# Performance work log

Hardware: AMD Instinct MI355X
Metric: run time of the kernel (lower is better)

## Reference

```python
import jax, jax.numpy as jnp
import numpy as np

N_NODES = 50000
N_EDGES = 800000
F_IN, D1, N_CLS = 128, 128, 64


def gcn_conv(x, W, b, src, dst, n):
    # x: [N, Fin] -> linear transform then normalized scatter-add aggregation
    h = x @ W  # [N, Fout]
    deg = jnp.zeros((n,), h.dtype).at[dst].add(jnp.ones((dst.shape[0],), h.dtype))
    dis = jnp.where(deg > 0, jax.lax.rsqrt(jnp.maximum(deg, 1.0)), 0.0)  # deg^-1/2, inf->0
    norm = dis[src] * dis[dst]  # [E_tot]
    msgs = norm[:, None] * h[src]  # gather source features, scale by sym norm
    out = jax.ops.segment_sum(msgs, dst, num_segments=n)  # scatter-add to targets
    return out + b


def setup_inputs() -> dict:
    key = jax.random.key(0)
    ks = jax.random.split(key, 6)
    x = jax.random.normal(ks[0], (N_NODES, F_IN), dtype=jnp.float32)
    edge_index = jax.random.randint(ks[1], (2, N_EDGES), 0, N_NODES, dtype=jnp.int64)
    W1 = jax.random.normal(ks[2], (F_IN, D1), dtype=jnp.float32) / np.sqrt(F_IN)
    b1 = jnp.zeros((D1,), dtype=jnp.float32)
    W2 = jax.random.normal(ks[3], (D1, N_CLS), dtype=jnp.float32) / np.sqrt(D1)
    b2 = jnp.zeros((N_CLS,), dtype=jnp.float32)
    return {"x": x, "edge_index": edge_index, "W1": W1, "b1": b1, "W2": W2, "b2": b2}


def reference(x, edge_index, W1, b1, W2, b2):
    n = x.shape[0]
    loops = jnp.arange(n, dtype=edge_index.dtype)
    src = jnp.concatenate([edge_index[0], loops])  # add self-loops (PyG default)
    dst = jnp.concatenate([edge_index[1], loops])
    h = gcn_conv(x, W1, b1, src, dst, n)
    h = jax.nn.relu(h)
    # F.dropout(training=self.training) is identity in eval mode
    out = gcn_conv(h, W2, b2, src, dst, n)
    return out
```

## Files before the change

kernel.cpp:

```cpp
#include <hip/hip_runtime.h>
#include <hip/hip_fp16.h>

#define NN 50000
#define NE 800000
#define CAP 64
#define CSTR 32
#define SLICE 6250

typedef unsigned int   u32;
typedef unsigned short u16;
typedef __attribute__((ext_vector_type(8))) short short8;
typedef __attribute__((ext_vector_type(4))) float f32x4;

__device__ inline u16 f2bf(float f) {
    u32 u = __float_as_uint(f);
    return (u16)((u + 0x7FFF + ((u >> 16) & 1)) >> 16);
}
__device__ inline float bfval(u16 h) { return __uint_as_float(((u32)h) << 16); }
__device__ inline float bf_lo(u32 u) { return __uint_as_float(u << 16); }
__device__ inline float bf_hi(u32 u) { return __uint_as_float(u & 0xFFFF0000u); }


__global__ __launch_bounds__(256) void build_ell(const int* __restrict__ ei,
                                                 int* __restrict__ cnt,
                                                 u16* __restrict__ ell) {
    const int s = blockIdx.x & 7;
    const int g = blockIdx.x >> 3;
    const int u = g * 256 + (int)threadIdx.x;
    const int lo = s * SLICE, hi = lo + SLICE;

    int dv[16], sv[16];
#pragma unroll
    for (int k = 0; k < 4; ++k) {
        int e0 = (u + k * 51200) * 4;
        if (e0 < NE) {
            *(int4*)&dv[k * 4] = *(const int4*)(ei + NE + e0);
            *(int4*)&sv[k * 4] = *(const int4*)(ei + e0);
        } else {
#pragma unroll
            for (int j = 0; j < 4; ++j) { dv[k * 4 + j] = -1; sv[k * 4 + j] = 0; }
        }
    }

    int pos[16];
#pragma unroll
    for (int k = 0; k < 16; ++k) {
        pos[k] = -1;
        if (dv[k] >= lo && dv[k] < hi)
            pos[k] = atomicAdd(&cnt[(size_t)dv[k] * CSTR], 1);
    }
#pragma unroll
    for (int k = 0; k < 16; ++k)
        if (pos[k] >= 0 && pos[k] < CAP)
            ell[(size_t)dv[k] * CAP + pos[k]] = (u16)sv[k];
}


__global__ __launch_bounds__(256) void prep_w(const float* __restrict__ W1,
                                              const float* __restrict__ W2,
                                              u16* __restrict__ W1h, u16* __restrict__ W1l,
                                              u16* __restrict__ W2h, u16* __restrict__ W2l,
                                              int* __restrict__ cnt) {
    int i = blockIdx.x * 256 + threadIdx.x;
    int4* c4 = (int4*)cnt;
    const int4 z = make_int4(0, 0, 0, 0);
    for (int v = i; v < NN * CSTR / 4; v += 32768) c4[v] = z;
    const float* W; u16 *Dh, *Dl; int NOUT, idx;
    if (i < 16384) { W = W1; Dh = W1h; Dl = W1l; NOUT = 128; idx = i; }
    else           { idx = i - 16384; if (idx >= 8192) return;
                     W = W2; Dh = W2h; Dl = W2l; NOUT = 64; }
    int j = idx & 7, l = (idx >> 3) & 63, kc = (idx >> 9) & 3, t = idx >> 11;
    int k = kc * 32 + (l >> 4) * 8 + j;
    int n = t * 16 + (l & 15);
    float w = W[k * NOUT + n];
    u16 h = f2bf(w);
    Dh[idx] = h;
    Dl[idx] = f2bf(w - bfval(h));
}


__global__ __launch_bounds__(256) void pack_edges(const u16* __restrict__ ell,
                                                  const int* __restrict__ cnt,
                                                  u32* __restrict__ epk,
                                                  u16* __restrict__ degm) {
    const int tid = threadIdx.x;
    const int node = blockIdx.x * 4 + (tid >> 6);
    if (node >= NN) return;
    const int lane = tid & 63;
    const int cr = cnt[(size_t)node * CSTR];
    const int ne = min(cr, 63);
    const float di = rsqrtf((float)(cr + 1));
    if (lane == 0) degm[node] = (u16)(ne + 1);
    if (lane > ne) return;
    int s; float nr;
    if (lane < ne) {
        s = (int)ell[(size_t)node * CAP + lane];
        nr = rsqrtf((float)(cnt[(size_t)s * CSTR] + 1)) * di;
    } else { s = node; nr = di * di; }
    epk[(size_t)node * CAP + lane] =
        (u32)s | ((u32)__half_as_ushort(__float2half_rn(nr)) << 16);
}


__global__ __launch_bounds__(256) void gemm1(const float* __restrict__ A,
                                             const u16* __restrict__ Wh,
                                             const u16* __restrict__ Wl,
                                             u16* __restrict__ C) {
    const int tid = threadIdx.x;
    const int w = tid >> 6, l = tid & 63;
    const int m = l & 15, q = l >> 4;

    int arow = blockIdx.x * 64 + w * 16 + m;
    const float* Ar = A + (size_t)min(arow, NN - 1) * 128;

    f32x4 acc[8] = {};
#pragma unroll
    for (int kc = 0; kc < 4; ++kc) {
        float p[8];
        *(float4*)&p[0] = *(const float4*)(Ar + kc * 32 + q * 8);
        *(float4*)&p[4] = *(const float4*)(Ar + kc * 32 + q * 8 + 4);
        short8 ah, al;
#pragma unroll
        for (int j = 0; j < 8; ++j) {
            u16 h = f2bf(p[j]);
            ah[j] = (short)h;
            al[j] = (short)f2bf(p[j] - bfval(h));
        }
#pragma unroll
        for (int t2 = 0; t2 < 8; ++t2) {
            size_t bo = ((size_t)(t2 * 4 + kc) * 64 + l) * 8;
            short8 bh = *(const short8*)(Wh + bo);
            short8 bl = *(const short8*)(Wl + bo);
            acc[t2] = __builtin_amdgcn_mfma_f32_16x16x32_bf16(ah, bh, acc[t2], 0, 0, 0);
            acc[t2] = __builtin_amdgcn_mfma_f32_16x16x32_bf16(al, bh, acc[t2], 0, 0, 0);
            acc[t2] = __builtin_amdgcn_mfma_f32_16x16x32_bf16(ah, bl, acc[t2], 0, 0, 0);
        }
    }
    int growbase = blockIdx.x * 64 + w * 16 + q * 4;
#pragma unroll
    for (int t2 = 0; t2 < 8; ++t2)
#pragma unroll
        for (int r = 0; r < 4; ++r) {
            int grow = growbase + r;
            if (grow < NN) C[(size_t)grow * 128 + t2 * 16 + m] = f2bf(acc[t2][r]);
        }
}


__global__ __launch_bounds__(256) void gemm2(const u16* __restrict__ A,
                                             const u16* __restrict__ Wh,
                                             const u16* __restrict__ Wl,
                                             u16* __restrict__ C) {
    const int tid = threadIdx.x;
    const int w = tid >> 6, l = tid & 63;
    const int m = l & 15, q = l >> 4;

    int arow = min(blockIdx.x * 64 + w * 16 + m, NN - 1);
    const u16* Ar = A + (size_t)arow * 128;

    f32x4 acc[4] = {};
#pragma unroll
    for (int kc = 0; kc < 4; ++kc) {
        short8 ah = *(const short8*)(Ar + kc * 32 + q * 8);
#pragma unroll
        for (int t2 = 0; t2 < 4; ++t2) {
            size_t bo = ((size_t)(t2 * 4 + kc) * 64 + l) * 8;
            short8 bh = *(const short8*)(Wh + bo);
            short8 bl = *(const short8*)(Wl + bo);
            acc[t2] = __builtin_amdgcn_mfma_f32_16x16x32_bf16(ah, bh, acc[t2], 0, 0, 0);
            acc[t2] = __builtin_amdgcn_mfma_f32_16x16x32_bf16(ah, bl, acc[t2], 0, 0, 0);
        }
    }
    int growbase = blockIdx.x * 64 + w * 16 + q * 4;
#pragma unroll
    for (int t2 = 0; t2 < 4; ++t2)
#pragma unroll
        for (int r = 0; r < 4; ++r) {
            int grow = growbase + r;
            if (grow < NN) C[(size_t)grow * 64 + t2 * 16 + m] = f2bf(acc[t2][r]);
        }
}


template <int F, bool RELU, bool OUTBF>
__global__ __launch_bounds__(256) void aggregate(const u16* __restrict__ H,
                                                 const u32* __restrict__ epk,
                                                 const u16* __restrict__ degm,
                                                 const float* __restrict__ bias,
                                                 void* __restrict__ outp) {
    const int tid = threadIdx.x;
    const int node = (int)((blockIdx.x * 256 + tid) >> 6);
    if (node >= NN) return;
    const int lane = tid & 63;

    const int m = (int)degm[node];
    u32 e = (lane < m) ? epk[(size_t)node * CAP + lane] : (u32)node;
    int   s_l = (int)(e & 0xFFFF);
    float n_l = (lane < m)
                    ? __half2float(__ushort_as_half((u16)(e >> 16)))
                    : 0.0f;

    constexpr int G = (F == 128) ? 4 : 8;
    constexpr int L = 64 / G;
    const int g = lane / L;
    const int ci = lane & (L - 1);

    const int mPad = (m + 2 * G - 1) & ~(2 * G - 1);

    float acc[8] = {0, 0, 0, 0, 0, 0, 0, 0};
    for (int j = 0; j < mPad; j += 2 * G) {
        int   sA = __shfl(s_l, j + g);
        float nA = __shfl(n_l, j + g);
        int   sB = __shfl(s_l, j + G + g);
        float nB = __shfl(n_l, j + G + g);
        uint4 vA = *(const uint4*)(H + (size_t)sA * F + ci * 8);
        uint4 vB = *(const uint4*)(H + (size_t)sB * F + ci * 8);
        acc[0] += nA * bf_lo(vA.x); acc[1] += nA * bf_hi(vA.x);
        acc[2] += nA * bf_lo(vA.y); acc[3] += nA * bf_hi(vA.y);
        acc[4] += nA * bf_lo(vA.z); acc[5] += nA * bf_hi(vA.z);
        acc[6] += nA * bf_lo(vA.w); acc[7] += nA * bf_hi(vA.w);
        acc[0] += nB * bf_lo(vB.x); acc[1] += nB * bf_hi(vB.x);
        acc[2] += nB * bf_lo(vB.y); acc[3] += nB * bf_hi(vB.y);
        acc[4] += nB * bf_lo(vB.z); acc[5] += nB * bf_hi(vB.z);
        acc[6] += nB * bf_lo(vB.w); acc[7] += nB * bf_hi(vB.w);
    }

#pragma unroll
    for (int i = 0; i < 8; ++i) {
        if (F == 64) acc[i] += __shfl_xor(acc[i], 8);
        acc[i] += __shfl_xor(acc[i], 16);
        acc[i] += __shfl_xor(acc[i], 32);
    }

    const int active = (F == 128) ? 32 : 16;
    if (lane < active) {
        int part, c0i;
        if (F == 128) { part = lane >> 4;       c0i = (lane & 15) * 8 + part * 4; }
        else          { part = (lane >> 3) & 1; c0i = (lane & 7) * 8 + part * 4; }
        float4 b4 = *(const float4*)(bias + c0i);
        float4 o = make_float4(acc[part * 4 + 0] + b4.x, acc[part * 4 + 1] + b4.y,
                               acc[part * 4 + 2] + b4.z, acc[part * 4 + 3] + b4.w);
        if (RELU) { o.x = fmaxf(o.x, 0.f); o.y = fmaxf(o.y, 0.f);
                    o.z = fmaxf(o.z, 0.f); o.w = fmaxf(o.w, 0.f); }
        if (OUTBF) {
            u16* out = (u16*)outp;
            *(ushort4*)(out + (size_t)node * F + c0i) =
                make_ushort4(f2bf(o.x), f2bf(o.y), f2bf(o.z), f2bf(o.w));
        } else {
            float* out = (float*)outp;
            *(float4*)(out + (size_t)node * F + c0i) = o;
        }
    }
}


extern "C" void kernel_launch(void* const* d_in, const int* in_sizes, int n_in,
                              void* d_out, int out_size, void* d_ws, size_t ws_size,
                              hipStream_t stream) {
    const float* x  = (const float*)d_in[0];
    const int*   ei = (const int*)d_in[1];
    const float* W1 = (const float*)d_in[2];
    const float* b1 = (const float*)d_in[3];
    const float* W2 = (const float*)d_in[4];
    const float* b2 = (const float*)d_in[5];
    float* out = (float*)d_out;

    char* ws = (char*)d_ws;
    size_t off = 0;
    int* cnt = (int*)ws;                     off += (size_t)NN * CSTR * 4;
    u16* ell = (u16*)(ws + off);             off += (size_t)NN * CAP * 2;
    off = (off + 255) & ~(size_t)255;
    u32* epk = (u32*)(ws + off);             off += (size_t)NN * CAP * 4;
    u16* degm = (u16*)(ws + off);            off += (size_t)NN * 2;
    off = (off + 255) & ~(size_t)255;
    u16* W1h = (u16*)(ws + off);             off += 16384 * 2;
    u16* W1l = (u16*)(ws + off);             off += 16384 * 2;
    u16* W2h = (u16*)(ws + off);             off += 8192 * 2;
    u16* W2l = (u16*)(ws + off);             off += 8192 * 2;
    off = (off + 255) & ~(size_t)255;
    u16* Hbf = (u16*)(ws + off);             off += (size_t)NN * 128 * 2;
    u16* Abf = (u16*)(ws + off);             off += (size_t)NN * 128 * 2;

    prep_w<<<128, 256, 0, stream>>>(W1, W2, W1h, W1l, W2h, W2l, cnt);
    build_ell<<<1600, 256, 0, stream>>>(ei, cnt, ell);
    pack_edges<<<12500, 256, 0, stream>>>(ell, cnt, epk, degm);

    gemm1<<<(NN + 63) / 64, 256, 0, stream>>>(x, W1h, W1l, Hbf);
    aggregate<128, true, true><<<(NN + 3) / 4, 256, 0, stream>>>(Hbf, epk, degm, b1, Abf);

    gemm2<<<(NN + 63) / 64, 256, 0, stream>>>(Abf, W2h, W2l, Hbf);
    aggregate<64, false, false><<<(NN + 3) / 4, 256, 0, stream>>>(Hbf, epk, degm, b2, out);
}
```

Measured before the change: 213.2 us.

## Fuse graph build with gemm1 and edge packing with layer-1 aggregation

Runs the independent ELL build and the first GEMM in one launch by splitting the grid into GEMM blocks and build blocks. The edge-packing pass is folded into the first aggregation kernel, which computes normalisation coefficients itself while still writing the packed edges for layer 2. The goal is to remove two kernel launches and one extra read of ell/cnt, and to let GEMM work overlap with the atomic-heavy build. In exchange the fused kernels carry more register pressure and a mixed per-block workload.

New measurement: 196.9 us. -7.6%, faster.

```diff
diff --git a/kernel.cpp b/kernel.cpp
--- a/kernel.cpp
+++ b/kernel.cpp
@@ -6,6 +6,7 @@
 #define CAP 64
 #define CSTR 32
 #define SLICE 6250
+#define GT1 782
 
 typedef unsigned int   u32;
 typedef unsigned short u16;
@@ -19,41 +20,6 @@
 __device__ inline float bfval(u16 h) { return __uint_as_float(((u32)h) << 16); }
 __device__ inline float bf_lo(u32 u) { return __uint_as_float(u << 16); }
 __device__ inline float bf_hi(u32 u) { return __uint_as_float(u & 0xFFFF0000u); }
-
-
-__global__ __launch_bounds__(256) void build_ell(const int* __restrict__ ei,
-                                                 int* __restrict__ cnt,
-                                                 u16* __restrict__ ell) {
-    const int s = blockIdx.x & 7;
-    const int g = blockIdx.x >> 3;
-    const int u = g * 256 + (int)threadIdx.x;
-    const int lo = s * SLICE, hi = lo + SLICE;
-
-    int dv[16], sv[16];
-#pragma unroll
-    for (int k = 0; k < 4; ++k) {
-        int e0 = (u + k * 51200) * 4;
-        if (e0 < NE) {
-            *(int4*)&dv[k * 4] = *(const int4*)(ei + NE + e0);
-            *(int4*)&sv[k * 4] = *(const int4*)(ei + e0);
-        } else {
-#pragma unroll
-            for (int j = 0; j < 4; ++j) { dv[k * 4 + j] = -1; sv[k * 4 + j] = 0; }
-        }
-    }
-
-    int pos[16];
-#pragma unroll
-    for (int k = 0; k < 16; ++k) {
-        pos[k] = -1;
-        if (dv[k] >= lo && dv[k] < hi)
-            pos[k] = atomicAdd(&cnt[(size_t)dv[k] * CSTR], 1);
-    }
-#pragma unroll
-    for (int k = 0; k < 16; ++k)
-        if (pos[k] >= 0 && pos[k] < CAP)
-            ell[(size_t)dv[k] * CAP + pos[k]] = (u16)sv[k];
-}
 
 
 __global__ __launch_bounds__(256) void prep_w(const float* __restrict__ W1,
@@ -79,38 +45,46 @@
 }
 
 
-__global__ __launch_bounds__(256) void pack_edges(const u16* __restrict__ ell,
-                                                  const int* __restrict__ cnt,
-                                                  u32* __restrict__ epk,
-                                                  u16* __restrict__ degm) {
-    const int tid = threadIdx.x;
-    const int node = blockIdx.x * 4 + (tid >> 6);
-    if (node >= NN) return;
-    const int lane = tid & 63;
-    const int cr = cnt[(size_t)node * CSTR];
-    const int ne = min(cr, 63);
-    const float di = rsqrtf((float)(cr + 1));
-    if (lane == 0) degm[node] = (u16)(ne + 1);
-    if (lane > ne) return;
-    int s; float nr;
-    if (lane < ne) {
-        s = (int)ell[(size_t)node * CAP + lane];
-        nr = rsqrtf((float)(cnt[(size_t)s * CSTR] + 1)) * di;
-    } else { s = node; nr = di * di; }
-    epk[(size_t)node * CAP + lane] =
-        (u32)s | ((u32)__half_as_ushort(__float2half_rn(nr)) << 16);
-}
-
-
-__global__ __launch_bounds__(256) void gemm1(const float* __restrict__ A,
-                                             const u16* __restrict__ Wh,
-                                             const u16* __restrict__ Wl,
-                                             u16* __restrict__ C) {
-    const int tid = threadIdx.x;
+__device__ void dev_build(int b, int tid, const int* __restrict__ ei,
+                          int* __restrict__ cnt, u16* __restrict__ ell) {
+    const int s = b & 7;
+    const int g = b >> 3;
+    const int u = g * 256 + tid;
+    const int lo = s * SLICE, hi = lo + SLICE;
+
+    int dv[16], sv[16];
+#pragma unroll
+    for (int k = 0; k < 4; ++k) {
+        int e0 = (u + k * 51200) * 4;
+        if (e0 < NE) {
+            *(int4*)&dv[k * 4] = *(const int4*)(ei + NE + e0);
+            *(int4*)&sv[k * 4] = *(const int4*)(ei + e0);
+        } else {
+#pragma unroll
+            for (int j = 0; j < 4; ++j) { dv[k * 4 + j] = -1; sv[k * 4 + j] = 0; }
+        }
+    }
+
+    int pos[16];
+#pragma unroll
+    for (int k = 0; k < 16; ++k) {
+        pos[k] = -1;
+        if (dv[k] >= lo && dv[k] < hi)
+            pos[k] = atomicAdd(&cnt[(size_t)dv[k] * CSTR], 1);
+    }
+#pragma unroll
+    for (int k = 0; k < 16; ++k)
+        if (pos[k] >= 0 && pos[k] < CAP)
+            ell[(size_t)dv[k] * CAP + pos[k]] = (u16)sv[k];
+}
+
+__device__ void dev_gemm1(int tile, int tid, const float* __restrict__ A,
+                          const u16* __restrict__ Wh, const u16* __restrict__ Wl,
+                          u16* __restrict__ C) {
     const int w = tid >> 6, l = tid & 63;
     const int m = l & 15, q = l >> 4;
 
-    int arow = blockIdx.x * 64 + w * 16 + m;
+    int arow = tile * 64 + w * 16 + m;
     const float* Ar = A + (size_t)min(arow, NN - 1) * 128;
 
     f32x4 acc[8] = {};
@@ -136,7 +110,7 @@
             acc[t2] = __builtin_amdgcn_mfma_f32_16x16x32_bf16(ah, bl, acc[t2], 0, 0, 0);
         }
     }
-    int growbase = blockIdx.x * 64 + w * 16 + q * 4;
+    int growbase = tile * 64 + w * 16 + q * 4;
 #pragma unroll
     for (int t2 = 0; t2 < 8; ++t2)
 #pragma unroll
@@ -146,75 +120,59 @@
         }
 }
 
-
-__global__ __launch_bounds__(256) void gemm2(const u16* __restrict__ A,
-                                             const u16* __restrict__ Wh,
-                                             const u16* __restrict__ Wl,
-                                             u16* __restrict__ C) {
-    const int tid = threadIdx.x;
-    const int w = tid >> 6, l = tid & 63;
-    const int m = l & 15, q = l >> 4;
-
-    int arow = min(blockIdx.x * 64 + w * 16 + m, NN - 1);
-    const u16* Ar = A + (size_t)arow * 128;
-
-    f32x4 acc[4] = {};
-#pragma unroll
-    for (int kc = 0; kc < 4; ++kc) {
-        short8 ah = *(const short8*)(Ar + kc * 32 + q * 8);
-#pragma unroll
-        for (int t2 = 0; t2 < 4; ++t2) {
-            size_t bo = ((size_t)(t2 * 4 + kc) * 64 + l) * 8;
-            short8 bh = *(const short8*)(Wh + bo);
-            short8 bl = *(const short8*)(Wl + bo);
-            acc[t2] = __builtin_amdgcn_mfma_f32_16x16x32_bf16(ah, bh, acc[t2], 0, 0, 0);
-            acc[t2] = __builtin_amdgcn_mfma_f32_16x16x32_bf16(ah, bl, acc[t2], 0, 0, 0);
-        }
-    }
-    int growbase = blockIdx.x * 64 + w * 16 + q * 4;
-#pragma unroll
-    for (int t2 = 0; t2 < 4; ++t2)
-#pragma unroll
-        for (int r = 0; r < 4; ++r) {
-            int grow = growbase + r;
-            if (grow < NN) C[(size_t)grow * 64 + t2 * 16 + m] = f2bf(acc[t2][r]);
-        }
-}
-
-
-template <int F, bool RELU, bool OUTBF>
-__global__ __launch_bounds__(256) void aggregate(const u16* __restrict__ H,
-                                                 const u32* __restrict__ epk,
-                                                 const u16* __restrict__ degm,
+__global__ __launch_bounds__(256) void k_build_gemm1(const int* __restrict__ ei,
+                                                     int* __restrict__ cnt,
+                                                     u16* __restrict__ ell,
+                                                     const float* __restrict__ x,
+                                                     const u16* __restrict__ W1h,
+                                                     const u16* __restrict__ W1l,
+                                                     u16* __restrict__ Hbf) {
+    const int b = blockIdx.x, tid = threadIdx.x;
+    if (b < GT1) dev_gemm1(b, tid, x, W1h, W1l, Hbf);
+    else         dev_build(b - GT1, tid, ei, cnt, ell);
+}
+
+
+__global__ __launch_bounds__(256) void agg1_pack(const u16* __restrict__ H,
+                                                 const u16* __restrict__ ell,
+                                                 const int* __restrict__ cnt,
+                                                 u32* __restrict__ epk,
+                                                 u16* __restrict__ degm,
                                                  const float* __restrict__ bias,
-                                                 void* __restrict__ outp) {
+                                                 u16* __restrict__ outp) {
     const int tid = threadIdx.x;
     const int node = (int)((blockIdx.x * 256 + tid) >> 6);
     if (node >= NN) return;
     const int lane = tid & 63;
 
-    const int m = (int)degm[node];
-    u32 e = (lane < m) ? epk[(size_t)node * CAP + lane] : (u32)node;
-    int   s_l = (int)(e & 0xFFFF);
-    float n_l = (lane < m)
-                    ? __half2float(__ushort_as_half((u16)(e >> 16)))
-                    : 0.0f;
-
-    constexpr int G = (F == 128) ? 4 : 8;
-    constexpr int L = 64 / G;
-    const int g = lane / L;
-    const int ci = lane & (L - 1);
-
-    const int mPad = (m + 2 * G - 1) & ~(2 * G - 1);
+    const int cr = cnt[(size_t)node * CSTR];
+    const int ne = min(cr, 63);
+    const int m = ne + 1;
+    const float di = rsqrtf((float)(cr + 1));
+    if (lane == 0) degm[node] = (u16)m;
+
+    int s_l; float n_l;
+    if (lane < ne) {
+        s_l = (int)ell[(size_t)node * CAP + lane];
+        n_l = rsqrtf((float)(cnt[(size_t)s_l * CSTR] + 1)) * di;
+    } else if (lane == ne) { s_l = node; n_l = di * di; }
+    else                   { s_l = node; n_l = 0.0f; }
+    if (lane < m)
+        epk[(size_t)node * CAP + lane] =
+            (u32)s_l | ((u32)__half_as_ushort(__float2half_rn(n_l)) << 16);
+
+    const int g = lane >> 4;
+    const int ci = lane & 15;
+    const int mPad = (m + 7) & ~7;
 
     float acc[8] = {0, 0, 0, 0, 0, 0, 0, 0};
-    for (int j = 0; j < mPad; j += 2 * G) {
+    for (int j = 0; j < mPad; j += 8) {
         int   sA = __shfl(s_l, j + g);
         float nA = __shfl(n_l, j + g);
-        int   sB = __shfl(s_l, j + G + g);
-        float nB = __shfl(n_l, j + G + g);
-        uint4 vA = *(const uint4*)(H + (size_t)sA * F + ci * 8);
-        uint4 vB = *(const uint4*)(H + (size_t)sB * F + ci * 8);
+        int   sB = __shfl(s_l, j + 4 + g);
+        float nB = __shfl(n_l, j + 4 + g);
+        uint4 vA = *(const uint4*)(H + (size_t)sA * 128 + ci * 8);
+        uint4 vB = *(const uint4*)(H + (size_t)sB * 128 + ci * 8);
         acc[0] += nA * bf_lo(vA.x); acc[1] += nA * bf_hi(vA.x);
         acc[2] += nA * bf_lo(vA.y); acc[3] += nA * bf_hi(vA.y);
         acc[4] += nA * bf_lo(vA.z); acc[5] += nA * bf_hi(vA.z);
@@ -227,29 +185,112 @@
 
 #pragma unroll
     for (int i = 0; i < 8; ++i) {
-        if (F == 64) acc[i] += __shfl_xor(acc[i], 8);
         acc[i] += __shfl_xor(acc[i], 16);
         acc[i] += __shfl_xor(acc[i], 32);
     }
 
-    const int active = (F == 128) ? 32 : 16;
-    if (lane < active) {
-        int part, c0i;
-        if (F == 128) { part = lane >> 4;       c0i = (lane & 15) * 8 + part * 4; }
-        else          { part = (lane >> 3) & 1; c0i = (lane & 7) * 8 + part * 4; }
+    if (lane < 32) {
+        int part = lane >> 4;
+        int c0i = (lane & 15) * 8 + part * 4;
         float4 b4 = *(const float4*)(bias + c0i);
         float4 o = make_float4(acc[part * 4 + 0] + b4.x, acc[part * 4 + 1] + b4.y,
                                acc[part * 4 + 2] + b4.z, acc[part * 4 + 3] + b4.w);
-        if (RELU) { o.x = fmaxf(o.x, 0.f); o.y = fmaxf(o.y, 0.f);
-                    o.z = fmaxf(o.z, 0.f); o.w = fmaxf(o.w, 0.f); }
-        if (OUTBF) {
-            u16* out = (u16*)outp;
-            *(ushort4*)(out + (size_t)node * F + c0i) =
-                make_ushort4(f2bf(o.x), f2bf(o.y), f2bf(o.z), f2bf(o.w));
-        } else {
-            float* out = (float*)outp;
-            *(float4*)(out + (size_t)node * F + c0i) = o;
-        }
+        o.x = fmaxf(o.x, 0.f); o.y = fmaxf(o.y, 0.f);
+        o.z = fmaxf(o.z, 0.f); o.w = fmaxf(o.w, 0.f);
+        *(ushort4*)(outp + (size_t)node * 128 + c0i) =
+            make_ushort4(f2bf(o.x), f2bf(o.y), f2bf(o.z), f2bf(o.w));
+    }
+}
+
+
+__global__ __launch_bounds__(256) void gemm2(const u16* __restrict__ A,
+                                             const u16* __restrict__ Wh,
+                                             const u16* __restrict__ Wl,
+                                             u16* __restrict__ C) {
+    const int tid = threadIdx.x;
+    const int w = tid >> 6, l = tid & 63;
+    const int m = l & 15, q = l >> 4;
+
+    int arow = min(blockIdx.x * 64 + w * 16 + m, NN - 1);
+    const u16* Ar = A + (size_t)arow * 128;
+
+    f32x4 acc[4] = {};
+#pragma unroll
+    for (int kc = 0; kc < 4; ++kc) {
+        short8 ah = *(const short8*)(Ar + kc * 32 + q * 8);
+#pragma unroll
+        for (int t2 = 0; t2 < 4; ++t2) {
+            size_t bo = ((size_t)(t2 * 4 + kc) * 64 + l) * 8;
+            short8 bh = *(const short8*)(Wh + bo);
+            short8 bl = *(const short8*)(Wl + bo);
+            acc[t2] = __builtin_amdgcn_mfma_f32_16x16x32_bf16(ah, bh, acc[t2], 0, 0, 0);
+            acc[t2] = __builtin_amdgcn_mfma_f32_16x16x32_bf16(ah, bl, acc[t2], 0, 0, 0);
+        }
+    }
+    int growbase = blockIdx.x * 64 + w * 16 + q * 4;
+#pragma unroll
+    for (int t2 = 0; t2 < 4; ++t2)
+#pragma unroll
+        for (int r = 0; r < 4; ++r) {
+            int grow = growbase + r;
+            if (grow < NN) C[(size_t)grow * 64 + t2 * 16 + m] = f2bf(acc[t2][r]);
+        }
+}
+
+
+__global__ __launch_bounds__(256) void agg2(const u16* __restrict__ H,
+                                            const u32* __restrict__ epk,
+                                            const u16* __restrict__ degm,
+                                            const float* __restrict__ bias,
+                                            float* __restrict__ outp) {
+    const int tid = threadIdx.x;
+    const int node = (int)((blockIdx.x * 256 + tid) >> 6);
+    if (node >= NN) return;
+    const int lane = tid & 63;
+
+    const int m = (int)degm[node];
+    u32 e = (lane < m) ? epk[(size_t)node * CAP + lane] : (u32)node;
+    int   s_l = (int)(e & 0xFFFF);
+    float n_l = (lane < m)
+                    ? __half2float(__ushort_as_half((u16)(e >> 16)))
+                    : 0.0f;
+
+    const int g = lane >> 3;
+    const int ci = lane & 7;
+    const int mPad = (m + 15) & ~15;
+
+    float acc[8] = {0, 0, 0, 0, 0, 0, 0, 0};
+    for (int j = 0; j < mPad; j += 16) {
+        int   sA = __shfl(s_l, j + g);
+        float nA = __shfl(n_l, j + g);
+        int   sB = __shfl(s_l, j + 8 + g);
+        float nB = __shfl(n_l, j + 8 + g);
+        uint4 vA = *(const uint4*)(H + (size_t)sA * 64 + ci * 8);
+        uint4 vB = *(const uint4*)(H + (size_t)sB * 64 + ci * 8);
+        acc[0] += nA * bf_lo(vA.x); acc[1] += nA * bf_hi(vA.x);
+        acc[2] += nA * bf_lo(vA.y); acc[3] += nA * bf_hi(vA.y);
+        acc[4] += nA * bf_lo(vA.z); acc[5] += nA * bf_hi(vA.z);
+        acc[6] += nA * bf_lo(vA.w); acc[7] += nA * bf_hi(vA.w);
+        acc[0] += nB * bf_lo(vB.x); acc[1] += nB * bf_hi(vB.x);
+        acc[2] += nB * bf_lo(vB.y); acc[3] += nB * bf_hi(vB.y);
+        acc[4] += nB * bf_lo(vB.z); acc[5] += nB * bf_hi(vB.z);
+        acc[6] += nB * bf_lo(vB.w); acc[7] += nB * bf_hi(vB.w);
+    }
+
+#pragma unroll
+    for (int i = 0; i < 8; ++i) {
+        acc[i] += __shfl_xor(acc[i], 8);
+        acc[i] += __shfl_xor(acc[i], 16);
+        acc[i] += __shfl_xor(acc[i], 32);
+    }
+
+    if (lane < 16) {
+        int part = (lane >> 3) & 1;
+        int c0i = (lane & 7) * 8 + part * 4;
+        float4 b4 = *(const float4*)(bias + c0i);
+        float4 o = make_float4(acc[part * 4 + 0] + b4.x, acc[part * 4 + 1] + b4.y,
+                               acc[part * 4 + 2] + b4.z, acc[part * 4 + 3] + b4.w);
+        *(float4*)(outp + (size_t)node * 64 + c0i) = o;
     }
 }
 
@@ -282,12 +323,8 @@
     u16* Abf = (u16*)(ws + off);             off += (size_t)NN * 128 * 2;
 
     prep_w<<<128, 256, 0, stream>>>(W1, W2, W1h, W1l, W2h, W2l, cnt);
-    build_ell<<<1600, 256, 0, stream>>>(ei, cnt, ell);
-    pack_edges<<<12500, 256, 0, stream>>>(ell, cnt, epk, degm);
-
-    gemm1<<<(NN + 63) / 64, 256, 0, stream>>>(x, W1h, W1l, Hbf);
-    aggregate<128, true, true><<<(NN + 3) / 4, 256, 0, stream>>>(Hbf, epk, degm, b1, Abf);
-
+    k_build_gemm1<<<GT1 + 1600, 256, 0, stream>>>(ei, cnt, ell, x, W1h, W1l, Hbf);
+    agg1_pack<<<(NN + 3) / 4, 256, 0, stream>>>(Hbf, ell, cnt, epk, degm, b1, Abf);
     gemm2<<<(NN + 63) / 64, 256, 0, stream>>>(Abf, W2h, W2l, Hbf);
-    aggregate<64, false, false><<<(NN + 3) / 4, 256, 0, stream>>>(Hbf, epk, degm, b2, out);
-}
+    agg2<<<(NN + 3) / 4, 256, 0, stream>>>(Hbf, epk, degm, b2, out);
+}
```
